# Kernel tuning notes

Measured on AMD Instinct MI355X. Metric: run time of the kernel, lower is better.

Reference implementation:

```python
import jax, jax.numpy as jnp
import numpy as np

N, FIN, H, C, D = 50000, 128, 4, 64, 4
E = 800000


def leaky_relu(x, slope):
    return jnp.where(x >= 0, x, slope * x)


def gat_layer(x, src, dst, W, A, att_src, att_dst, bias):
    # x: [N, Fin]; W: [Fin, H*C]; A: [Fin, H*D]; att_*: [H, D]; bias: [C]
    n = x.shape[0]
    h = (x @ W).reshape(n, H, -1)          # [N, H, C] message features
    a = (x @ A).reshape(n, H, -1)          # [N, H, D] attention features
    alpha_src = jnp.einsum('nhd,hd->nh', a, att_src)   # [N, H]
    alpha_dst = jnp.einsum('nhd,hd->nh', a, att_dst)   # [N, H]
    e = leaky_relu(alpha_src[src] + alpha_dst[dst], 0.2)  # [E, H]
    # edge softmax over incoming edges of each destination node
    m = jax.ops.segment_max(e, dst, num_segments=n)       # [N, H]
    ex = jnp.exp(e - m[dst])                               # [E, H]
    denom = jax.ops.segment_sum(ex, dst, num_segments=n)  # [N, H]
    w = ex / denom[dst]                                    # [E, H]
    msg = h[src] * w[..., None]                            # [E, H, C]
    out = jax.ops.segment_sum(msg, dst, num_segments=n)   # [N, H, C]
    return out.mean(axis=1) + bias                         # head-average -> [N, C]


def setup_inputs() -> dict:
    key = jax.random.key(0)
    ks = jax.random.split(key, 12)
    x = jax.random.normal(ks[0], (N, FIN), dtype=jnp.float32)
    edge_index = jax.random.randint(ks[1], (2, E), 0, N, dtype=jnp.int64)
    s = 0.05
    return {
        'x': x,
        'edge_index': edge_index,
        'W1': jax.random.normal(ks[2], (FIN, H * C), dtype=jnp.float32) * s,
        'A1': jax.random.normal(ks[3], (FIN, H * D), dtype=jnp.float32) * s,
        'att_src1': jax.random.normal(ks[4], (H, D), dtype=jnp.float32) * s,
        'att_dst1': jax.random.normal(ks[5], (H, D), dtype=jnp.float32) * s,
        'b1': jnp.zeros((C,), dtype=jnp.float32),
        'W2': jax.random.normal(ks[6], (C, H * C), dtype=jnp.float32) * s,
        'A2': jax.random.normal(ks[7], (C, H * D), dtype=jnp.float32) * s,
        'att_src2': jax.random.normal(ks[8], (H, D), dtype=jnp.float32) * s,
        'att_dst2': jax.random.normal(ks[9], (H, D), dtype=jnp.float32) * s,
        'b2': jnp.zeros((C,), dtype=jnp.float32),
    }


def reference(x, edge_index, W1, A1, att_src1, att_dst1, b1, W2, A2, att_src2, att_dst2, b2):
    src, dst = edge_index[0], edge_index[1]
    x = gat_layer(x, src, dst, W1, A1, att_src1, att_dst1, b1)
    x = leaky_relu(x, 0.1)
    x = gat_layer(x, src, dst, W2, A2, att_src2, att_dst2, b2)
    x = leaky_relu(x, 0.1)
    return x
```

## Files before the change

kernel.cpp:

```cpp
#include <hip/hip_runtime.h>


#define N_NODES 50000
#define N_EDGES 800000
#define CAP 64
#define NB_SC4 782
#define NB_NODE1 782

typedef __attribute__((ext_vector_type(8))) short short8;
typedef __attribute__((ext_vector_type(8))) _Float16 f16x8;
typedef __attribute__((ext_vector_type(2))) _Float16 f16x2;
typedef __attribute__((ext_vector_type(4))) float f32x4;
typedef __attribute__((ext_vector_type(8))) unsigned short ushort8;
typedef __attribute__((ext_vector_type(4))) unsigned short us4v;

__device__ __forceinline__ float bf2f(unsigned short u){
  return __uint_as_float(((unsigned int)u) << 16);
}
__device__ __forceinline__ unsigned short f2bf(float f){
  unsigned int u = __float_as_uint(f);
  u = (u + 0x7FFFu + ((u >> 16) & 1u)) >> 16;
  return (unsigned short)u;
}
__device__ __forceinline__ float ldf(const void* p, int i, bool bf){
  return bf ? bf2f(((const unsigned short*)p)[i]) : ((const float*)p)[i];
}
__device__ __forceinline__ float rdlane(float v, int lane){
  return __uint_as_float(__builtin_amdgcn_readlane(__float_as_uint(v), lane));
}

struct SetupPtrs {
  const void *W1, *A1, *aS1, *aD1, *b1, *W2, *A2, *aS2, *aD2, *b2, *x;
};

__global__ __launch_bounds__(256) void k_setup(SetupPtrs S,
    _Float16* __restrict__ Wb1f, _Float16* __restrict__ Wb2f,
    unsigned short* __restrict__ Bsd1f, unsigned short* __restrict__ Bsd2f,
    float* __restrict__ bc1, float* __restrict__ bc2,
    int* __restrict__ flag)
{
  __shared__ int sbf;
  const int tid = threadIdx.x;
  if (tid < 64){
    unsigned int w = ((const unsigned int*)S.x)[tid] & 0xFFFFu;
    unsigned int e = (w >> 7) & 0xFFu;
    bool hit = (e >= 100u && e <= 135u);
    unsigned long long m = __ballot(hit);
    if (tid == 0) sbf = (__popcll(m) > 40) ? 1 : 0;
  }
  __syncthreads();
  const bool bf = (sbf != 0);
  const int bw = blockIdx.x;
  if (bw < 128){
    int t = bw * 256 + tid;
    int j = t & 7, lane = (t >> 3) & 63, kt = (t >> 9) & 15, nt = t >> 13;
    int q = kt * 32 + (lane >> 4) * 8 + j;
    int c = nt * 16 + (lane & 15);
    int h = q >> 7, f = q & 127;
    Wb1f[t] = (_Float16)(0.25f * ldf(S.W1, f * 256 + h * 64 + c, bf));
  } else if (bw < 192){
    int t = (bw - 128) * 256 + tid;
    int j = t & 7, lane = (t >> 3) & 63, kt = (t >> 9) & 7, nt = t >> 12;
    int q = kt * 32 + (lane >> 4) * 8 + j;
    int c = nt * 16 + (lane & 15);
    int h = q >> 6, f = q & 63;
    Wb2f[t] = (_Float16)(0.25f * ldf(S.W2, f * 256 + h * 64 + c, bf));
  } else if (bw < 200){
    int t = (bw - 192) * 256 + tid;
    int j = t & 7, lane = (t >> 3) & 63, kt = t >> 9;
    int k = kt * 32 + (lane >> 4) * 8 + j;
    int c = lane & 15;
    float v = 0.f;
    if (c < 4){
      for (int dd = 0; dd < 4; ++dd)
        v += ldf(S.A1, k * 16 + c * 4 + dd, bf) * ldf(S.aS1, c * 4 + dd, bf);
    } else if (c < 8){
      int h = c - 4;
      for (int dd = 0; dd < 4; ++dd)
        v += ldf(S.A1, k * 16 + h * 4 + dd, bf) * ldf(S.aD1, h * 4 + dd, bf);
    }
    Bsd1f[t] = f2bf(v);
  } else if (bw < 204){
    int t = (bw - 200) * 256 + tid;
    int j = t & 7, lane = (t >> 3) & 63, kt = t >> 9;
    int k = kt * 32 + (lane >> 4) * 8 + j;
    int c = lane & 15;
    float v = 0.f;
    if (c < 4){
      for (int dd = 0; dd < 4; ++dd)
        v += ldf(S.A2, k * 16 + c * 4 + dd, bf) * ldf(S.aS2, c * 4 + dd, bf);
    } else if (c < 8){
      int h = c - 4;
      for (int dd = 0; dd < 4; ++dd)
        v += ldf(S.A2, k * 16 + h * 4 + dd, bf) * ldf(S.aD2, h * 4 + dd, bf);
    }
    Bsd2f[t] = f2bf(v);
  } else {
    if (tid < 64)       bc1[tid] = ldf(S.b1, tid, bf);
    else if (tid < 128) bc2[tid - 64] = ldf(S.b2, tid - 64, bf);
    else if (tid == 128) *flag = bf ? 1 : 0;
  }
}


__device__ __forceinline__ void nodeA_body(int nblk, int tid,
    const void* __restrict__ xin_, const unsigned short* __restrict__ Bsdf,
    float* __restrict__ alpha_s, float* __restrict__ alpha_d,
    const int* __restrict__ flag)
{
  const int F = 128, STR = F + 8, KT = 4, CH = F / 8;
  __shared__ unsigned short xs[64 * 136];
  const int base = nblk * 64;
  const bool bf = (*flag != 0);
  for (int v = tid; v < 64 * CH; v += 256){
    int row = v / CH, c8 = v % CH;
    int node = base + row; if (node >= N_NODES) node = N_NODES - 1;
    size_t g = (size_t)node * F + c8 * 8;
    ushort8 u;
    if (bf){
      u = *(const ushort8*)((const unsigned short*)xin_ + g);
    } else {
      const float* xf = (const float*)xin_ + g;
      float4 f0 = *(const float4*)xf, f1 = *(const float4*)(xf + 4);
      u[0]=f2bf(f0.x); u[1]=f2bf(f0.y); u[2]=f2bf(f0.z); u[3]=f2bf(f0.w);
      u[4]=f2bf(f1.x); u[5]=f2bf(f1.y); u[6]=f2bf(f1.z); u[7]=f2bf(f1.w);
    }
    *(ushort8*)&xs[row * STR + c8 * 8] = u;
  }
  __syncthreads();

  const int wave = tid >> 6, l = tid & 63;
  const int quad = l >> 4, m = l & 15;
  const int wbase = base + wave * 16;

  f32x4 aacc = (f32x4)0.f;
  #pragma unroll
  for (int kt = 0; kt < KT; ++kt){
    short8 af = *(const short8*)&xs[(wave * 16 + m) * STR + kt * 32 + quad * 8];
    short8 sdfrag = *(const short8*)(Bsdf + ((size_t)kt * 64 + l) * 8);
    aacc = __builtin_amdgcn_mfma_f32_16x16x32_bf16(af, sdfrag, aacc, 0, 0, 0);
  }
  if (m < 8){
    float* dstp = (m < 4) ? alpha_s : alpha_d;
    int hh = m & 3;
    #pragma unroll
    for (int r = 0; r < 4; ++r){
      int node = wbase + quad * 4 + r;
      if (node < N_NODES) dstp[node * 4 + hh] = aacc[r];
    }
  }
}


__global__ __launch_bounds__(256) void k_scatter_nodeA1(
    const int* __restrict__ src, const int* __restrict__ dst,
    int* __restrict__ fill, unsigned short* __restrict__ csr,
    const void* __restrict__ xin_, const unsigned short* __restrict__ Bsdf,
    float* __restrict__ alpha_s, float* __restrict__ alpha_d,
    const int* __restrict__ flag)
{
  const int b = blockIdx.x, tid = threadIdx.x;
  if (b < NB_SC4){
    const int ebase = b * 1024 + tid;
    int d[4], s[4];
    #pragma unroll
    for (int i = 0; i < 4; ++i){
      int e = ebase + i * 256;
      bool ok = (e < N_EDGES);
      d[i] = ok ? dst[e] : -1;
      s[i] = ok ? src[e] : 0;
    }
    #pragma unroll
    for (int i = 0; i < 4; ++i){
      if (d[i] >= 0){
        int r = atomicAdd(&fill[d[i]], 1);
        if (r < CAP) csr[((unsigned)d[i] << 6) + r] = (unsigned short)s[i];
      }
    }
    return;
  }
  nodeA_body(b - NB_SC4, tid, xin_, Bsdf, alpha_s, alpha_d, flag);
}


template<bool BF, int STR>
__device__ __forceinline__ void aggr_phase1_u128(const void* __restrict__ xg,
    const float* __restrict__ alpha_s, const float* __restrict__ alpha_d,
    const int* __restrict__ fill, const unsigned short* __restrict__ csr,
    _Float16* __restrict__ ylds, int base, int w, int l)
{
  const int h = l >> 4;
  #pragma unroll 1
  for (int r = 0; r < 4; ++r){
    const int n = base + w * 4 + r;
    const float adv = alpha_d[n * 4 + h];
    float den = 0.f;
    float acc[4][2];
    #pragma unroll
    for (int hh = 0; hh < 4; ++hh){ acc[hh][0] = 0.f; acc[hh][1] = 0.f; }

    int cnt = fill[n]; if (cnt > CAP) cnt = CAP;
    const unsigned short* cp = csr + ((unsigned)n << 6);
    int p = 0;
    for (; p + 8 <= cnt; p += 8){
      ushort8 s8 = *(const ushort8*)(cp + p);
      float a[8];
      float lo[8], hi[8];
      #pragma unroll
      for (int i = 0; i < 8; ++i){
        unsigned s = s8[i];
        a[i] = alpha_s[s * 4 + h];
        if (BF){
          unsigned xv = *(const unsigned int*)((const unsigned short*)xg + (size_t)s * 128 + 2 * l);
          lo[i] = bf2f((unsigned short)(xv & 0xFFFFu));
          hi[i] = bf2f((unsigned short)(xv >> 16));
        } else {
          const float* xf = (const float*)xg + (size_t)s * 128 + 2 * l;
          lo[i] = xf[0]; hi[i] = xf[1];
        }
      }
      #pragma unroll
      for (int i = 0; i < 8; ++i){
        float e = a[i] + adv; e = fmaxf(e, 0.2f * e); float wt = __expf(e);
        den += wt;
        float w0 = rdlane(wt, 0),  w1 = rdlane(wt, 16);
        float w2 = rdlane(wt, 32), w3 = rdlane(wt, 48);
        acc[0][0] += w0 * lo[i]; acc[0][1] += w0 * hi[i];
        acc[1][0] += w1 * lo[i]; acc[1][1] += w1 * hi[i];
        acc[2][0] += w2 * lo[i]; acc[2][1] += w2 * hi[i];
        acc[3][0] += w3 * lo[i]; acc[3][1] += w3 * hi[i];
      }
    }
    if (p + 4 <= cnt){
      ushort4 s4 = *(const ushort4*)(cp + p);
      unsigned ss[4] = {s4.x, s4.y, s4.z, s4.w};
      float a[4], lo[4], hi[4];
      #pragma unroll
      for (int i = 0; i < 4; ++i){
        a[i] = alpha_s[ss[i] * 4 + h];
        if (BF){
          unsigned xv = *(const unsigned int*)((const unsigned short*)xg + (size_t)ss[i] * 128 + 2 * l);
          lo[i] = bf2f((unsigned short)(xv & 0xFFFFu));
          hi[i] = bf2f((unsigned short)(xv >> 16));
        } else {
          const float* xf = (const float*)xg + (size_t)ss[i] * 128 + 2 * l;
          lo[i] = xf[0]; hi[i] = xf[1];
        }
      }
      #pragma unroll
      for (int i = 0; i < 4; ++i){
        float e = a[i] + adv; e = fmaxf(e, 0.2f * e); float wt = __expf(e);
        den += wt;
        float w0 = rdlane(wt, 0),  w1 = rdlane(wt, 16);
        float w2 = rdlane(wt, 32), w3 = rdlane(wt, 48);
        acc[0][0] += w0 * lo[i]; acc[0][1] += w0 * hi[i];
        acc[1][0] += w1 * lo[i]; acc[1][1] += w1 * hi[i];
        acc[2][0] += w2 * lo[i]; acc[2][1] += w2 * hi[i];
        acc[3][0] += w3 * lo[i]; acc[3][1] += w3 * hi[i];
      }
      p += 4;
    }
    for (; p < cnt; ++p){
      unsigned s = cp[p];
      float a = alpha_s[s * 4 + h];
      float lo, hi;
      if (BF){
        unsigned xv = *(const unsigned int*)((const unsigned short*)xg + (size_t)s * 128 + 2 * l);
        lo = bf2f((unsigned short)(xv & 0xFFFFu));
        hi = bf2f((unsigned short)(xv >> 16));
      } else {
        const float* xf = (const float*)xg + (size_t)s * 128 + 2 * l;
        lo = xf[0]; hi = xf[1];
      }
      float e = a + adv; e = fmaxf(e, 0.2f * e); float wt = __expf(e);
      den += wt;
      float w0 = rdlane(wt, 0),  w1 = rdlane(wt, 16);
      float w2 = rdlane(wt, 32), w3 = rdlane(wt, 48);
      acc[0][0] += w0 * lo; acc[0][1] += w0 * hi;
      acc[1][0] += w1 * lo; acc[1][1] += w1 * hi;
      acc[2][0] += w2 * lo; acc[2][1] += w2 * hi;
      acc[3][0] += w3 * lo; acc[3][1] += w3 * hi;
    }
    float d0 = rdlane(den, 0),  d1 = rdlane(den, 16);
    float d2 = rdlane(den, 32), d3 = rdlane(den, 48);
    float rh0 = (d0 > 0.f) ? (1.f / d0) : 0.f;
    float rh1 = (d1 > 0.f) ? (1.f / d1) : 0.f;
    float rh2 = (d2 > 0.f) ? (1.f / d2) : 0.f;
    float rh3 = (d3 > 0.f) ? (1.f / d3) : 0.f;
    const int row = w * 4 + r;
    _Float16* yp = &ylds[row * STR + 2 * l];
    *(f16x2*)(yp +   0) = (f16x2){(_Float16)(acc[0][0] * rh0), (_Float16)(acc[0][1] * rh0)};
    *(f16x2*)(yp + 128) = (f16x2){(_Float16)(acc[1][0] * rh1), (_Float16)(acc[1][1] * rh1)};
    *(f16x2*)(yp + 256) = (f16x2){(_Float16)(acc[2][0] * rh2), (_Float16)(acc[2][1] * rh2)};
    *(f16x2*)(yp + 384) = (f16x2){(_Float16)(acc[3][0] * rh3), (_Float16)(acc[3][1] * rh3)};
  }
}

template<int STR>
__device__ __forceinline__ void aggr_phase1_u64(const unsigned short* __restrict__ xg,
    const float* __restrict__ alpha_s, const float* __restrict__ alpha_d,
    const int* __restrict__ fill, const unsigned short* __restrict__ csr,
    _Float16* __restrict__ ylds, int base, int w, int l)
{
  const int h = l >> 4;
  #pragma unroll 1
  for (int r = 0; r < 4; ++r){
    const int n = base + w * 4 + r;
    const float adv = alpha_d[n * 4 + h];
    float den = 0.f;
    float acc[4] = {0.f, 0.f, 0.f, 0.f};

    int cnt = fill[n]; if (cnt > CAP) cnt = CAP;
    const unsigned short* cp = csr + ((unsigned)n << 6);
    int p = 0;
    for (; p + 8 <= cnt; p += 8){
      ushort8 s8 = *(const ushort8*)(cp + p);
      float a[8], xv[8];
      #pragma unroll
      for (int i = 0; i < 8; ++i){
        unsigned s = s8[i];
        a[i] = alpha_s[s * 4 + h];
        xv[i] = bf2f(xg[(size_t)s * 64 + l]);
      }
      #pragma unroll
      for (int i = 0; i < 8; ++i){
        float e = a[i] + adv; e = fmaxf(e, 0.2f * e); float wt = __expf(e);
        den += wt;
        float w0 = rdlane(wt, 0),  w1 = rdlane(wt, 16);
        float w2 = rdlane(wt, 32), w3 = rdlane(wt, 48);
        acc[0] += w0 * xv[i]; acc[1] += w1 * xv[i];
        acc[2] += w2 * xv[i]; acc[3] += w3 * xv[i];
      }
    }
    if (p + 4 <= cnt){
      ushort4 s4 = *(const ushort4*)(cp + p);
      unsigned ss[4] = {s4.x, s4.y, s4.z, s4.w};
      float a[4], xv[4];
      #pragma unroll
      for (int i = 0; i < 4; ++i){
        a[i] = alpha_s[ss[i] * 4 + h];
        xv[i] = bf2f(xg[(size_t)ss[i] * 64 + l]);
      }
      #pragma unroll
      for (int i = 0; i < 4; ++i){
        float e = a[i] + adv; e = fmaxf(e, 0.2f * e); float wt = __expf(e);
        den += wt;
        float w0 = rdlane(wt, 0),  w1 = rdlane(wt, 16);
        float w2 = rdlane(wt, 32), w3 = rdlane(wt, 48);
        acc[0] += w0 * xv[i]; acc[1] += w1 * xv[i];
        acc[2] += w2 * xv[i]; acc[3] += w3 * xv[i];
      }
      p += 4;
    }
    for (; p < cnt; ++p){
      unsigned s = cp[p];
      float a = alpha_s[s * 4 + h];
      float xv = bf2f(xg[(size_t)s * 64 + l]);
      float e = a + adv; e = fmaxf(e, 0.2f * e); float wt = __expf(e);
      den += wt;
      float w0 = rdlane(wt, 0),  w1 = rdlane(wt, 16);
      float w2 = rdlane(wt, 32), w3 = rdlane(wt, 48);
      acc[0] += w0 * xv; acc[1] += w1 * xv;
      acc[2] += w2 * xv; acc[3] += w3 * xv;
    }
    float d0 = rdlane(den, 0),  d1 = rdlane(den, 16);
    float d2 = rdlane(den, 32), d3 = rdlane(den, 48);
    float rh0 = (d0 > 0.f) ? (1.f / d0) : 0.f;
    float rh1 = (d1 > 0.f) ? (1.f / d1) : 0.f;
    float rh2 = (d2 > 0.f) ? (1.f / d2) : 0.f;
    float rh3 = (d3 > 0.f) ? (1.f / d3) : 0.f;
    const int row = w * 4 + r;
    _Float16* yp = &ylds[row * STR + l];
    yp[0]   = (_Float16)(acc[0] * rh0);
    yp[64]  = (_Float16)(acc[1] * rh1);
    yp[128] = (_Float16)(acc[2] * rh2);
    yp[192] = (_Float16)(acc[3] * rh3);
  }
}

template<int FIN, int MODE>
__global__ __launch_bounds__(256) void k_aggrX(
    const void* __restrict__ xg,
    const float* __restrict__ alpha_s, const float* __restrict__ alpha_d,
    const int* __restrict__ fill, const unsigned short* __restrict__ csr,
    const _Float16* __restrict__ Wf,
    const float* __restrict__ bias, void* __restrict__ out,
    const int* __restrict__ flag,
    const unsigned short* __restrict__ Bsd2f,
    float* __restrict__ as2, float* __restrict__ ad2)
{
  const int K = 4 * FIN, KT = K / 32, STR = K + 8;
  __shared__ _Float16 ylds[16 * (4 * FIN + 8)];
  __shared__ unsigned short x2t[16 * 72];
  const int tid = threadIdx.x, w = tid >> 6, l = tid & 63;
  const int base = blockIdx.x * 16;

  if (FIN == 128){
    if (MODE == 0 && *flag == 0)
      aggr_phase1_u128<false, STR>(xg, alpha_s, alpha_d, fill, csr, ylds, base, w, l);
    else
      aggr_phase1_u128<true,  STR>(xg, alpha_s, alpha_d, fill, csr, ylds, base, w, l);
  } else {
    aggr_phase1_u64<STR>((const unsigned short*)xg, alpha_s, alpha_d, fill, csr, ylds, base, w, l);
  }
  __syncthreads();

  const int quad = l >> 4, m = l & 15;
  const int nt = w;
  f32x4 cacc = (f32x4)0.f;
  #pragma unroll
  for (int kt = 0; kt < KT; ++kt){
    f16x8 av = *(const f16x8*)&ylds[m * STR + kt * 32 + quad * 8];
    f16x8 bv = *(const f16x8*)(Wf + ((size_t)(nt * KT + kt) * 64 + l) * 8);
    cacc = __builtin_amdgcn_mfma_f32_16x16x32_f16(av, bv, cacc, 0, 0, 0);
  }
  const int c = nt * 16 + m;
  const float bs = bias[c];
  #pragma unroll
  for (int r2 = 0; r2 < 4; ++r2){
    int node = base + quad * 4 + r2;
    float v = cacc[r2] + bs;
    v = fmaxf(v, 0.1f * v);
    if (MODE == 0){
      unsigned short o = f2bf(v);
      ((unsigned short*)out)[(size_t)node * 64 + c] = o;
      x2t[(quad * 4 + r2) * 72 + c] = o;
    } else {
      if (*flag) ((unsigned short*)out)[(size_t)node * 64 + c] = f2bf(v);
      else       ((float*)out)[(size_t)node * 64 + c] = v;
    }
  }

  if (MODE == 0){
    __syncthreads();
    if (w == 0){
      f32x4 aacc = (f32x4)0.f;
      #pragma unroll
      for (int kt = 0; kt < 2; ++kt){
        short8 af = *(const short8*)&x2t[m * 72 + kt * 32 + quad * 8];
        short8 sd = *(const short8*)(Bsd2f + ((size_t)kt * 64 + l) * 8);
        aacc = __builtin_amdgcn_mfma_f32_16x16x32_bf16(af, sd, aacc, 0, 0, 0);
      }
      if (m < 8){
        float* dstp = (m < 4) ? as2 : ad2;
        int hh = m & 3;
        #pragma unroll
        for (int r = 0; r < 4; ++r){
          int node = base + quad * 4 + r;
          dstp[node * 4 + hh] = aacc[r];
        }
      }
    }
  }
}


extern "C" void kernel_launch(void* const* d_in, const int* in_sizes, int n_in,
                              void* d_out, int out_size, void* d_ws, size_t ws_size,
                              hipStream_t stream)
{
  const void* x  = d_in[0];
  const int* ei  = (const int*)d_in[1];
  const int* src = ei;
  const int* dst = ei + N_EDGES;

  char* ws = (char*)d_ws;
  unsigned short* csr = (unsigned short*)(ws);
  unsigned short* x2  = (unsigned short*)(ws + 6400000);
  float* as_    = (float*)(ws + 12800000);
  float* ad_    = (float*)(ws + 13600000);
  float* as2_   = (float*)(ws + 14400000);
  float* ad2_   = (float*)(ws + 15200000);
  int*   fill   = (int*)  (ws + 16000000);
  _Float16* Wb1f = (_Float16*)(ws + 16200000);
  _Float16* Wb2f = (_Float16*)(ws + 16265536);
  unsigned short* Bsd1f = (unsigned short*)(ws + 16298304);
  unsigned short* Bsd2f = (unsigned short*)(ws + 16302400);
  float* bc1    = (float*)(ws + 16304448);
  float* bc2    = (float*)(ws + 16304704);
  int*   flag   = (int*)  (ws + 16304960);

  hipMemsetAsync(fill, 0, N_NODES * sizeof(int), stream);

  SetupPtrs S;
  S.W1 = d_in[2];  S.A1 = d_in[3];  S.aS1 = d_in[4];  S.aD1 = d_in[5];  S.b1 = d_in[6];
  S.W2 = d_in[7];  S.A2 = d_in[8];  S.aS2 = d_in[9];  S.aD2 = d_in[10]; S.b2 = d_in[11];
  S.x  = x;
  k_setup<<<205, 256, 0, stream>>>(S, Wb1f, Wb2f, Bsd1f, Bsd2f, bc1, bc2, flag);

  k_scatter_nodeA1<<<NB_SC4 + NB_NODE1, 256, 0, stream>>>(
      src, dst, fill, csr, x, Bsd1f, as_, ad_, flag);

  k_aggrX<128, 0><<<N_NODES / 16, 256, 0, stream>>>(
      x, as_, ad_, fill, csr, Wb1f, bc1, x2, flag, Bsd2f, as2_, ad2_);

  k_aggrX<64, 1><<<N_NODES / 16, 256, 0, stream>>>(
      x2, as2_, ad2_, fill, csr, Wb2f, bc2, d_out, flag, Bsd2f, as2_, ad2_);
}
```

Baseline: 277.1 us.

## Spread edges across lane groups with vectorized gathers and shuffle reduction

The per-node aggregation changes from one edge at a time across the whole wavefront to several edges at once, one per lane group. In layer 1 each group of 16 lanes takes an edge and in layer 2 each group of 8 lanes does, with 16-byte vector loads of source features and all four heads' attention weights computed per lane. Partial sums are then combined with xor shuffles, replacing per-edge readlane broadcasts. This aims to raise memory-level parallelism and cut scalar broadcast overhead, at the cost of more accumulator registers and a cross-lane reduction per node. The separate memset of the fill counters is also folded into the setup kernel to save a launch.

```diff
diff --git a/kernel.cpp b/kernel.cpp
--- a/kernel.cpp
+++ b/kernel.cpp
@@ -25,9 +25,6 @@
 __device__ __forceinline__ float ldf(const void* p, int i, bool bf){
   return bf ? bf2f(((const unsigned short*)p)[i]) : ((const float*)p)[i];
 }
-__device__ __forceinline__ float rdlane(float v, int lane){
-  return __uint_as_float(__builtin_amdgcn_readlane(__float_as_uint(v), lane));
-}
 
 struct SetupPtrs {
   const void *W1, *A1, *aS1, *aD1, *b1, *W2, *A2, *aS2, *aD2, *b2, *x;
@@ -37,10 +34,15 @@
     _Float16* __restrict__ Wb1f, _Float16* __restrict__ Wb2f,
     unsigned short* __restrict__ Bsd1f, unsigned short* __restrict__ Bsd2f,
     float* __restrict__ bc1, float* __restrict__ bc2,
-    int* __restrict__ flag)
+    int* __restrict__ flag, int* __restrict__ fill)
 {
   __shared__ int sbf;
   const int tid = threadIdx.x;
+  const int bw = blockIdx.x;
+  {
+    int gid = bw * 256 + tid;
+    if (gid < N_NODES) fill[gid] = 0;
+  }
   if (tid < 64){
     unsigned int w = ((const unsigned int*)S.x)[tid] & 0xFFFFu;
     unsigned int e = (w >> 7) & 0xFFu;
@@ -50,7 +52,6 @@
   }
   __syncthreads();
   const bool bf = (sbf != 0);
-  const int bw = blockIdx.x;
   if (bw < 128){
     int t = bw * 256 + tid;
     int j = t & 7, lane = (t >> 3) & 63, kt = (t >> 9) & 15, nt = t >> 13;
@@ -189,110 +190,85 @@
     const int* __restrict__ fill, const unsigned short* __restrict__ csr,
     _Float16* __restrict__ ylds, int base, int w, int l)
 {
-  const int h = l >> 4;
+  const int g = l >> 4;
+  const int sub = l & 15;
   #pragma unroll 1
   for (int r = 0; r < 4; ++r){
     const int n = base + w * 4 + r;
-    const float adv = alpha_d[n * 4 + h];
-    float den = 0.f;
-    float acc[4][2];
-    #pragma unroll
-    for (int hh = 0; hh < 4; ++hh){ acc[hh][0] = 0.f; acc[hh][1] = 0.f; }
+    const float4 ad4 = *(const float4*)(alpha_d + (size_t)n * 4);
+    float den[4] = {0.f, 0.f, 0.f, 0.f};
+    float acc[4][8];
+    #pragma unroll
+    for (int h = 0; h < 4; ++h)
+      #pragma unroll
+      for (int j = 0; j < 8; ++j) acc[h][j] = 0.f;
 
     int cnt = fill[n]; if (cnt > CAP) cnt = CAP;
     const unsigned short* cp = csr + ((unsigned)n << 6);
-    int p = 0;
-    for (; p + 8 <= cnt; p += 8){
-      ushort8 s8 = *(const ushort8*)(cp + p);
-      float a[8];
-      float lo[8], hi[8];
-      #pragma unroll
-      for (int i = 0; i < 8; ++i){
-        unsigned s = s8[i];
-        a[i] = alpha_s[s * 4 + h];
-        if (BF){
-          unsigned xv = *(const unsigned int*)((const unsigned short*)xg + (size_t)s * 128 + 2 * l);
-          lo[i] = bf2f((unsigned short)(xv & 0xFFFFu));
-          hi[i] = bf2f((unsigned short)(xv >> 16));
-        } else {
-          const float* xf = (const float*)xg + (size_t)s * 128 + 2 * l;
-          lo[i] = xf[0]; hi[i] = xf[1];
-        }
-      }
-      #pragma unroll
-      for (int i = 0; i < 8; ++i){
-        float e = a[i] + adv; e = fmaxf(e, 0.2f * e); float wt = __expf(e);
-        den += wt;
-        float w0 = rdlane(wt, 0),  w1 = rdlane(wt, 16);
-        float w2 = rdlane(wt, 32), w3 = rdlane(wt, 48);
-        acc[0][0] += w0 * lo[i]; acc[0][1] += w0 * hi[i];
-        acc[1][0] += w1 * lo[i]; acc[1][1] += w1 * hi[i];
-        acc[2][0] += w2 * lo[i]; acc[2][1] += w2 * hi[i];
-        acc[3][0] += w3 * lo[i]; acc[3][1] += w3 * hi[i];
-      }
-    }
-    if (p + 4 <= cnt){
-      ushort4 s4 = *(const ushort4*)(cp + p);
-      unsigned ss[4] = {s4.x, s4.y, s4.z, s4.w};
-      float a[4], lo[4], hi[4];
-      #pragma unroll
-      for (int i = 0; i < 4; ++i){
-        a[i] = alpha_s[ss[i] * 4 + h];
-        if (BF){
-          unsigned xv = *(const unsigned int*)((const unsigned short*)xg + (size_t)ss[i] * 128 + 2 * l);
-          lo[i] = bf2f((unsigned short)(xv & 0xFFFFu));
-          hi[i] = bf2f((unsigned short)(xv >> 16));
-        } else {
-          const float* xf = (const float*)xg + (size_t)ss[i] * 128 + 2 * l;
-          lo[i] = xf[0]; hi[i] = xf[1];
-        }
-      }
-      #pragma unroll
-      for (int i = 0; i < 4; ++i){
-        float e = a[i] + adv; e = fmaxf(e, 0.2f * e); float wt = __expf(e);
-        den += wt;
-        float w0 = rdlane(wt, 0),  w1 = rdlane(wt, 16);
-        float w2 = rdlane(wt, 32), w3 = rdlane(wt, 48);
-        acc[0][0] += w0 * lo[i]; acc[0][1] += w0 * hi[i];
-        acc[1][0] += w1 * lo[i]; acc[1][1] += w1 * hi[i];
-        acc[2][0] += w2 * lo[i]; acc[2][1] += w2 * hi[i];
-        acc[3][0] += w3 * lo[i]; acc[3][1] += w3 * hi[i];
-      }
-      p += 4;
-    }
-    for (; p < cnt; ++p){
-      unsigned s = cp[p];
-      float a = alpha_s[s * 4 + h];
-      float lo, hi;
+    for (int p = 0; p < cnt; p += 8){
+      int eA = p + g;      bool vA = (eA < cnt); int iA = vA ? eA : 0;
+      int eB = p + 4 + g;  bool vB = (eB < cnt); int iB = vB ? eB : 0;
+      unsigned sA = cp[iA], sB = cp[iB];
+      float xA[8], xB[8];
       if (BF){
-        unsigned xv = *(const unsigned int*)((const unsigned short*)xg + (size_t)s * 128 + 2 * l);
-        lo = bf2f((unsigned short)(xv & 0xFFFFu));
-        hi = bf2f((unsigned short)(xv >> 16));
+        ushort8 uA = *(const ushort8*)((const unsigned short*)xg + (size_t)sA * 128 + sub * 8);
+        ushort8 uB = *(const ushort8*)((const unsigned short*)xg + (size_t)sB * 128 + sub * 8);
+        #pragma unroll
+        for (int j = 0; j < 8; ++j){ xA[j] = bf2f(uA[j]); xB[j] = bf2f(uB[j]); }
       } else {
-        const float* xf = (const float*)xg + (size_t)s * 128 + 2 * l;
-        lo = xf[0]; hi = xf[1];
-      }
-      float e = a + adv; e = fmaxf(e, 0.2f * e); float wt = __expf(e);
-      den += wt;
-      float w0 = rdlane(wt, 0),  w1 = rdlane(wt, 16);
-      float w2 = rdlane(wt, 32), w3 = rdlane(wt, 48);
-      acc[0][0] += w0 * lo; acc[0][1] += w0 * hi;
-      acc[1][0] += w1 * lo; acc[1][1] += w1 * hi;
-      acc[2][0] += w2 * lo; acc[2][1] += w2 * hi;
-      acc[3][0] += w3 * lo; acc[3][1] += w3 * hi;
-    }
-    float d0 = rdlane(den, 0),  d1 = rdlane(den, 16);
-    float d2 = rdlane(den, 32), d3 = rdlane(den, 48);
-    float rh0 = (d0 > 0.f) ? (1.f / d0) : 0.f;
-    float rh1 = (d1 > 0.f) ? (1.f / d1) : 0.f;
-    float rh2 = (d2 > 0.f) ? (1.f / d2) : 0.f;
-    float rh3 = (d3 > 0.f) ? (1.f / d3) : 0.f;
-    const int row = w * 4 + r;
-    _Float16* yp = &ylds[row * STR + 2 * l];
-    *(f16x2*)(yp +   0) = (f16x2){(_Float16)(acc[0][0] * rh0), (_Float16)(acc[0][1] * rh0)};
-    *(f16x2*)(yp + 128) = (f16x2){(_Float16)(acc[1][0] * rh1), (_Float16)(acc[1][1] * rh1)};
-    *(f16x2*)(yp + 256) = (f16x2){(_Float16)(acc[2][0] * rh2), (_Float16)(acc[2][1] * rh2)};
-    *(f16x2*)(yp + 384) = (f16x2){(_Float16)(acc[3][0] * rh3), (_Float16)(acc[3][1] * rh3)};
+        const float* pA = (const float*)xg + (size_t)sA * 128 + sub * 8;
+        const float* pB = (const float*)xg + (size_t)sB * 128 + sub * 8;
+        float4 a0 = *(const float4*)pA, a1 = *(const float4*)(pA + 4);
+        float4 b0 = *(const float4*)pB, b1 = *(const float4*)(pB + 4);
+        xA[0]=a0.x; xA[1]=a0.y; xA[2]=a0.z; xA[3]=a0.w;
+        xA[4]=a1.x; xA[5]=a1.y; xA[6]=a1.z; xA[7]=a1.w;
+        xB[0]=b0.x; xB[1]=b0.y; xB[2]=b0.z; xB[3]=b0.w;
+        xB[4]=b1.x; xB[5]=b1.y; xB[6]=b1.z; xB[7]=b1.w;
+      }
+      float4 aA = *(const float4*)(alpha_s + (size_t)sA * 4);
+      float4 aB = *(const float4*)(alpha_s + (size_t)sB * 4);
+      float wA[4], wB[4];
+      { float e = aA.x + ad4.x; e = fmaxf(e, 0.2f * e); wA[0] = vA ? __expf(e) : 0.f; }
+      { float e = aA.y + ad4.y; e = fmaxf(e, 0.2f * e); wA[1] = vA ? __expf(e) : 0.f; }
+      { float e = aA.z + ad4.z; e = fmaxf(e, 0.2f * e); wA[2] = vA ? __expf(e) : 0.f; }
+      { float e = aA.w + ad4.w; e = fmaxf(e, 0.2f * e); wA[3] = vA ? __expf(e) : 0.f; }
+      { float e = aB.x + ad4.x; e = fmaxf(e, 0.2f * e); wB[0] = vB ? __expf(e) : 0.f; }
+      { float e = aB.y + ad4.y; e = fmaxf(e, 0.2f * e); wB[1] = vB ? __expf(e) : 0.f; }
+      { float e = aB.z + ad4.z; e = fmaxf(e, 0.2f * e); wB[2] = vB ? __expf(e) : 0.f; }
+      { float e = aB.w + ad4.w; e = fmaxf(e, 0.2f * e); wB[3] = vB ? __expf(e) : 0.f; }
+      #pragma unroll
+      for (int h = 0; h < 4; ++h){
+        den[h] += wA[h] + wB[h];
+        #pragma unroll
+        for (int j = 0; j < 8; ++j)
+          acc[h][j] += wA[h] * xA[j] + wB[h] * xB[j];
+      }
+    }
+    #pragma unroll
+    for (int h = 0; h < 4; ++h){
+      #pragma unroll
+      for (int j = 0; j < 8; ++j){
+        float v = acc[h][j];
+        v += __shfl_xor(v, 16);
+        v += __shfl_xor(v, 32);
+        acc[h][j] = v;
+      }
+      float d = den[h];
+      d += __shfl_xor(d, 16);
+      d += __shfl_xor(d, 32);
+      den[h] = d;
+    }
+    if (g == 0){
+      const int row = w * 4 + r;
+      #pragma unroll
+      for (int h = 0; h < 4; ++h){
+        float rh = (den[h] > 0.f) ? (1.f / den[h]) : 0.f;
+        f16x8 o;
+        #pragma unroll
+        for (int j = 0; j < 8; ++j) o[j] = (_Float16)(acc[h][j] * rh);
+        *(f16x8*)&ylds[row * STR + h * 128 + sub * 8] = o;
+      }
+    }
   }
 }
 
@@ -302,79 +278,78 @@
     const int* __restrict__ fill, const unsigned short* __restrict__ csr,
     _Float16* __restrict__ ylds, int base, int w, int l)
 {
-  const int h = l >> 4;
+  const int g = l >> 3;
+  const int sub = l & 7;
   #pragma unroll 1
   for (int r = 0; r < 4; ++r){
     const int n = base + w * 4 + r;
-    const float adv = alpha_d[n * 4 + h];
-    float den = 0.f;
-    float acc[4] = {0.f, 0.f, 0.f, 0.f};
+    const float4 ad4 = *(const float4*)(alpha_d + (size_t)n * 4);
+    float den[4] = {0.f, 0.f, 0.f, 0.f};
+    float acc[4][8];
+    #pragma unroll
+    for (int h = 0; h < 4; ++h)
+      #pragma unroll
+      for (int j = 0; j < 8; ++j) acc[h][j] = 0.f;
 
     int cnt = fill[n]; if (cnt > CAP) cnt = CAP;
     const unsigned short* cp = csr + ((unsigned)n << 6);
-    int p = 0;
-    for (; p + 8 <= cnt; p += 8){
-      ushort8 s8 = *(const ushort8*)(cp + p);
-      float a[8], xv[8];
-      #pragma unroll
-      for (int i = 0; i < 8; ++i){
-        unsigned s = s8[i];
-        a[i] = alpha_s[s * 4 + h];
-        xv[i] = bf2f(xg[(size_t)s * 64 + l]);
-      }
-      #pragma unroll
-      for (int i = 0; i < 8; ++i){
-        float e = a[i] + adv; e = fmaxf(e, 0.2f * e); float wt = __expf(e);
-        den += wt;
-        float w0 = rdlane(wt, 0),  w1 = rdlane(wt, 16);
-        float w2 = rdlane(wt, 32), w3 = rdlane(wt, 48);
-        acc[0] += w0 * xv[i]; acc[1] += w1 * xv[i];
-        acc[2] += w2 * xv[i]; acc[3] += w3 * xv[i];
-      }
-    }
-    if (p + 4 <= cnt){
-      ushort4 s4 = *(const ushort4*)(cp + p);
-      unsigned ss[4] = {s4.x, s4.y, s4.z, s4.w};
-      float a[4], xv[4];
-      #pragma unroll
-      for (int i = 0; i < 4; ++i){
-        a[i] = alpha_s[ss[i] * 4 + h];
-        xv[i] = bf2f(xg[(size_t)ss[i] * 64 + l]);
-      }
-      #pragma unroll
-      for (int i = 0; i < 4; ++i){
-        float e = a[i] + adv; e = fmaxf(e, 0.2f * e); float wt = __expf(e);
-        den += wt;
-        float w0 = rdlane(wt, 0),  w1 = rdlane(wt, 16);
-        float w2 = rdlane(wt, 32), w3 = rdlane(wt, 48);
-        acc[0] += w0 * xv[i]; acc[1] += w1 * xv[i];
-        acc[2] += w2 * xv[i]; acc[3] += w3 * xv[i];
-      }
-      p += 4;
-    }
-    for (; p < cnt; ++p){
-      unsigned s = cp[p];
-      float a = alpha_s[s * 4 + h];
-      float xv = bf2f(xg[(size_t)s * 64 + l]);
-      float e = a + adv; e = fmaxf(e, 0.2f * e); float wt = __expf(e);
-      den += wt;
-      float w0 = rdlane(wt, 0),  w1 = rdlane(wt, 16);
-      float w2 = rdlane(wt, 32), w3 = rdlane(wt, 48);
-      acc[0] += w0 * xv; acc[1] += w1 * xv;
-      acc[2] += w2 * xv; acc[3] += w3 * xv;
-    }
-    float d0 = rdlane(den, 0),  d1 = rdlane(den, 16);
-    float d2 = rdlane(den, 32), d3 = rdlane(den, 48);
-    float rh0 = (d0 > 0.f) ? (1.f / d0) : 0.f;
-    float rh1 = (d1 > 0.f) ? (1.f / d1) : 0.f;
-    float rh2 = (d2 > 0.f) ? (1.f / d2) : 0.f;
-    float rh3 = (d3 > 0.f) ? (1.f / d3) : 0.f;
-    const int row = w * 4 + r;
-    _Float16* yp = &ylds[row * STR + l];
-    yp[0]   = (_Float16)(acc[0] * rh0);
-    yp[64]  = (_Float16)(acc[1] * rh1);
-    yp[128] = (_Float16)(acc[2] * rh2);
-    yp[192] = (_Float16)(acc[3] * rh3);
+    for (int p = 0; p < cnt; p += 16){
+      int eA = p + g;      bool vA = (eA < cnt); int iA = vA ? eA : 0;
+      int eB = p + 8 + g;  bool vB = (eB < cnt); int iB = vB ? eB : 0;
+      unsigned sA = cp[iA], sB = cp[iB];
+      float xA[8], xB[8];
+      {
+        ushort8 uA = *(const ushort8*)(xg + (size_t)sA * 64 + sub * 8);
+        ushort8 uB = *(const ushort8*)(xg + (size_t)sB * 64 + sub * 8);
+        #pragma unroll
+        for (int j = 0; j < 8; ++j){ xA[j] = bf2f(uA[j]); xB[j] = bf2f(uB[j]); }
+      }
+      float4 aA = *(const float4*)(alpha_s + (size_t)sA * 4);
+      float4 aB = *(const float4*)(alpha_s + (size_t)sB * 4);
+      float wA[4], wB[4];
+      { float e = aA.x + ad4.x; e = fmaxf(e, 0.2f * e); wA[0] = vA ? __expf(e) : 0.f; }
+      { float e = aA.y + ad4.y; e = fmaxf(e, 0.2f * e); wA[1] = vA ? __expf(e) : 0.f; }
+      { float e = aA.z + ad4.z; e = fmaxf(e, 0.2f * e); wA[2] = vA ? __expf(e) : 0.f; }
+      { float e = aA.w + ad4.w; e = fmaxf(e, 0.2f * e); wA[3] = vA ? __expf(e) : 0.f; }
+      { float e = aB.x + ad4.x; e = fmaxf(e, 0.2f * e); wB[0] = vB ? __expf(e) : 0.f; }
+      { float e = aB.y + ad4.y; e = fmaxf(e, 0.2f * e); wB[1] = vB ? __expf(e) : 0.f; }
+      { float e = aB.z + ad4.z; e = fmaxf(e, 0.2f * e); wB[2] = vB ? __expf(e) : 0.f; }
+      { float e = aB.w + ad4.w; e = fmaxf(e, 0.2f * e); wB[3] = vB ? __expf(e) : 0.f; }
+      #pragma unroll
+      for (int h = 0; h < 4; ++h){
+        den[h] += wA[h] + wB[h];
+        #pragma unroll
+        for (int j = 0; j < 8; ++j)
+          acc[h][j] += wA[h] * xA[j] + wB[h] * xB[j];
+      }
+    }
+    #pragma unroll
+    for (int h = 0; h < 4; ++h){
+      #pragma unroll
+      for (int j = 0; j < 8; ++j){
+        float v = acc[h][j];
+        v += __shfl_xor(v, 8);
+        v += __shfl_xor(v, 16);
+        v += __shfl_xor(v, 32);
+        acc[h][j] = v;
+      }
+      float d = den[h];
+      d += __shfl_xor(d, 8);
+      d += __shfl_xor(d, 16);
+      d += __shfl_xor(d, 32);
+      den[h] = d;
+    }
+    if (g == 0){
+      const int row = w * 4 + r;
+      #pragma unroll
+      for (int h = 0; h < 4; ++h){
+        float rh = (den[h] > 0.f) ? (1.f / den[h]) : 0.f;
+        f16x8 o;
+        #pragma unroll
+        for (int j = 0; j < 8; ++j) o[j] = (_Float16)(acc[h][j] * rh);
+        *(f16x8*)&ylds[row * STR + h * 64 + sub * 8] = o;
+      }
+    }
   }
 }
 
@@ -480,13 +455,11 @@
   float* bc2    = (float*)(ws + 16304704);
   int*   flag   = (int*)  (ws + 16304960);
 
-  hipMemsetAsync(fill, 0, N_NODES * sizeof(int), stream);
-
   SetupPtrs S;
   S.W1 = d_in[2];  S.A1 = d_in[3];  S.aS1 = d_in[4];  S.aD1 = d_in[5];  S.b1 = d_in[6];
   S.W2 = d_in[7];  S.A2 = d_in[8];  S.aS2 = d_in[9];  S.aD2 = d_in[10]; S.b2 = d_in[11];
   S.x  = x;
-  k_setup<<<205, 256, 0, stream>>>(S, Wb1f, Wb2f, Bsd1f, Bsd2f, bc1, bc2, flag);
+  k_setup<<<205, 256, 0, stream>>>(S, Wb1f, Wb2f, Bsd1f, Bsd2f, bc1, bc2, flag, fill);
 
   k_scatter_nodeA1<<<NB_SC4 + NB_NODE1, 256, 0, stream>>>(
       src, dst, fill, csr, x, Bsd1f, as_, ad_, flag);
```

Result: slower. 310.4 us (+12.0%).
